# Kernel tuning notes

Measured on AMD Instinct MI355X. Metric: run time of the kernel, lower is better.

Reference implementation:

```python
import jax, jax.numpy as jnp
import numpy as np

EPS = 1e-4


def setup_inputs() -> dict:
    key = jax.random.key(0)
    k1, k2, k3 = jax.random.split(key, 3)
    B, L, M, D = 4, 8192, 4096, 1024
    hidden_states = jax.random.normal(k1, (B, M, D), dtype=jnp.float32)
    boundary_mask = (jax.random.uniform(k2, (B, L)) < 0.45).at[:, 0].set(True)
    boundary_prob = jax.nn.softmax(jax.random.normal(k3, (B, L, 2)), axis=-1)
    mask = jnp.ones((B, L), dtype=bool)
    return {
        "hidden_states": hidden_states,
        "boundary_prob": boundary_prob,
        "boundary_mask": boundary_mask,
        "mask": mask,
    }


def _dechunk(hidden_states, boundary_prob, boundary_mask):
    B, M, D = hidden_states.shape
    L = boundary_mask.shape[1]
    # stable-sort boundary tokens to the front (argsort of offset token idx)
    p_full = jnp.clip(boundary_prob[..., -1].astype(jnp.float32), EPS, 1.0 - EPS)  # [B,L]
    token_idx = jnp.arange(L, dtype=jnp.int32)[None, :] + (~boundary_mask).astype(jnp.int32) * L
    seq_sorted = jnp.argsort(token_idx, axis=1)[:, :M]  # [B,M]
    p = jnp.take_along_axis(p_full, seq_sorted, axis=1)  # [B,M]

    dt = jnp.log(1.0 / (1.0 - p)).astype(jnp.bfloat16)  # bf16 as in module dtype
    x = (hidden_states / dt[..., None].astype(jnp.float32)).astype(jnp.bfloat16)  # [B,M,D]

    # mamba_chunk_scan_combined with A=-1, dstate=1, B=p, C=1 reduces to the
    # linear recurrence h_t = exp(-dt_t) * h_{t-1} + dt_t * p_t * x_t ; y_t = h_t
    dt_f = dt.astype(jnp.float32)
    a = jnp.exp(-dt_f)[..., None]  # [B,M,1] decay = (1-p)
    b = (dt_f * p)[..., None] * x.astype(jnp.float32)  # [B,M,D]

    def combine(e1, e2):
        a1, b1 = e1
        a2, b2 = e2
        return (a1 * a2, a2 * b1 + b2)

    _, h = jax.lax.associative_scan(combine, (a, b), axis=1)  # h: [B,M,D]
    out = h.astype(jnp.bfloat16)  # kernel output dtype follows x (bf16)

    # scatter back: every token reads the state of its (most recent) chunk
    plug_back_idx = jnp.clip(jnp.cumsum(boundary_mask.astype(jnp.int32), axis=1) - 1, 0, M - 1)  # [B,L]
    out_full = jnp.take_along_axis(out, plug_back_idx[..., None], axis=1)  # [B,L,D]
    return out_full.astype(jnp.float32)  # back to original dtype


def reference(hidden_states, boundary_prob, boundary_mask, mask):
    # mask only participates in an assertion in the torch module
    return _dechunk(hidden_states, boundary_prob, boundary_mask)
```

## Files before the change

kernel.cpp:

```cpp
#include <hip/hip_runtime.h>
#include <hip/hip_bf16.h>
#include <math.h>

#define B_ 4
#define L_ 8192
#define M_ 4096
#define D_ 1024
#define CHUNK_ 32
#define NCC_ 128
#define EPS_ 1e-4f

typedef float f32x4 __attribute__((ext_vector_type(4)));

__device__ __forceinline__ float bf16rf(float x) {
  unsigned u = __float_as_uint(x);
  u += 0x7FFFu + ((u >> 16) & 1u);
  u &= 0xFFFF0000u;
  return __uint_as_float(u);
}

__device__ __forceinline__ bool mask_at(const void* mb, int fmt, int i) {
  if (fmt == 0) return ((const unsigned char*)mb)[i] != 0;
  if (fmt == 1) return ((const int*)mb)[i] != 0;
  return ((const float*)mb)[i] != 0.0f;
}

__device__ __forceinline__ void chunk_scal(const float* __restrict__ p_sorted,
                                           int b, int c, int tid,
                                           float4* s_scal) {
  if (tid < CHUNK_) {
    float p = p_sorted[b * M_ + c * CHUNK_ + tid];
    p = fminf(fmaxf(p, EPS_), 1.0f - EPS_);
    float dtf = bf16rf(logf(1.0f / (1.0f - p)));
    s_scal[tid] = make_float4(expf(-dtf), dtf * p, 1.0f / dtf, 0.0f);
  }
}

__global__ void __launch_bounds__(1024)
k_prep(const float* __restrict__ bprob,
       const void* __restrict__ bmask,
       float* __restrict__ p_sorted,
       int* __restrict__ rowstart) {
  const int b = blockIdx.x;
  const int tid = threadIdx.x;
  const int lane = tid & 63, wid = tid >> 6;
  __shared__ int s_flags[2];
  __shared__ int s_wsum[17];

  if (tid < 2) s_flags[tid] = 0;
  __syncthreads();
  {
    const unsigned* mw = (const unsigned*)bmask;
    unsigned f0 = 0, f1 = 0;
    for (int i = tid; i < 8192; i += 1024) {
      unsigned v = mw[i];
      f0 |= v & 0xFFu;
      f1 |= v & 0xFF00u;
    }
    if (f1) s_flags[0] = 1;
    if (f0) s_flags[1] = 1;
  }
  __syncthreads();
  const int fmt = s_flags[0] ? 0 : (s_flags[1] ? 1 : 2);

  const int base_l = tid * (L_ / 1024);
  bool mloc[L_ / 1024];
  int cnt = 0;
#pragma unroll
  for (int j = 0; j < L_ / 1024; ++j) {
    mloc[j] = mask_at(bmask, fmt, b * L_ + base_l + j);
    cnt += mloc[j] ? 1 : 0;
  }
  int incl = cnt;
#pragma unroll
  for (int off = 1; off < 64; off <<= 1) {
    int t = __shfl_up(incl, off);
    if (lane >= off) incl += t;
  }
  if (lane == 63) s_wsum[wid] = incl;
  __syncthreads();
  if (tid == 0) {
    int acc = 0;
#pragma unroll
    for (int w = 0; w < 16; ++w) { int t = s_wsum[w]; s_wsum[w] = acc; acc += t; }
    s_wsum[16] = acc;
  }
  for (int r = tid; r <= M_; r += 1024) rowstart[b * (M_ + 1) + r] = L_;
  __syncthreads();
  const int excl = s_wsum[wid] + incl - cnt;
  const int nb = s_wsum[16];

  int run = excl;
#pragma unroll
  for (int j = 0; j < L_ / 1024; ++j) {
    int l = base_l + j;
    bool mb = mloc[j];
    int pos = mb ? run : (nb + (l - run));
    run += mb ? 1 : 0;
    if (pos < M_) {
      p_sorted[b * M_ + pos] = bprob[((size_t)(b * L_ + l)) * 2 + 1];
      if (mb) rowstart[b * (M_ + 1) + pos] = l;
    }
  }
}

__global__ void __launch_bounds__(256)
k_scanA(const float* __restrict__ hidden,
        const float* __restrict__ p_sorted,
        const int* __restrict__ rowstart,
        float* __restrict__ carry,
        float* __restrict__ Achunk) {
  const int c = blockIdx.x, b = blockIdx.y;
  const int tid = threadIdx.x;
  if (rowstart[b * (M_ + 1) + c * CHUNK_] >= L_) return;
  __shared__ float4 s_scal[CHUNK_];
  chunk_scal(p_sorted, b, c, tid, s_scal);
  __syncthreads();
  if (tid == 0) {
    float cp = 1.0f;
#pragma unroll
    for (int m = 0; m < CHUNK_; ++m) cp *= s_scal[m].x;
    Achunk[b * NCC_ + c] = cp;
  }
  const int d4 = tid * 4;
  const float* __restrict__ hp =
      hidden + ((size_t)(b * M_ + c * CHUNK_)) * D_ + d4;
  float hx = 0.f, hy = 0.f, hz = 0.f, hw = 0.f;
#pragma unroll
  for (int m = 0; m < CHUNK_; ++m) {
    const float4 s = s_scal[m];
    const float4 x = *(const float4*)(hp + (size_t)m * D_);
    hx = fmaf(s.x, hx, s.y * bf16rf(x.x * s.z));
    hy = fmaf(s.x, hy, s.y * bf16rf(x.y * s.z));
    hz = fmaf(s.x, hz, s.y * bf16rf(x.z * s.z));
    hw = fmaf(s.x, hw, s.y * bf16rf(x.w * s.z));
  }
  *(float4*)(carry + ((size_t)(b * NCC_ + c)) * D_ + d4) =
      make_float4(hx, hy, hz, hw);
}

__global__ void __launch_bounds__(64)
k_scanB(float* __restrict__ carry, const float* __restrict__ Achunk) {
  const int chain = blockIdx.x * 64 + threadIdx.x;
  const int bb = chain >> 10, dd = chain & 1023;
  const float* __restrict__ Ab = Achunk + bb * NCC_;
  float S = 0.0f;
  for (int g = 0; g < NCC_ / 16; ++g) {
    float v[16], A[16];
#pragma unroll
    for (int j = 0; j < 16; ++j)
      v[j] = carry[((size_t)(bb * NCC_ + g * 16 + j)) * D_ + dd];
#pragma unroll
    for (int j = 0; j < 16; ++j) A[j] = Ab[g * 16 + j];
#pragma unroll
    for (int j = 0; j < 16; ++j) { S = fmaf(A[j], S, v[j]); v[j] = S; }
#pragma unroll
    for (int j = 0; j < 16; ++j)
      carry[((size_t)(bb * NCC_ + g * 16 + j)) * D_ + dd] = v[j];
  }
}

__global__ void __launch_bounds__(256)
k_scanC(const float* __restrict__ hidden,
        const float* __restrict__ p_sorted,
        const int* __restrict__ rowstart,
        const float* __restrict__ carry,
        float* __restrict__ out) {
  const int c = blockIdx.x, b = blockIdx.y;
  const int tid = threadIdx.x;
  const int d4 = tid * 4;
  __shared__ float4 s_scal[CHUNK_];
  __shared__ int    s_rs[CHUNK_ + 1];

  float hx = 0.f, hy = 0.f, hz = 0.f, hw = 0.f;
  if (c > 0) {
    const float4 ci =
        *(const float4*)(carry + ((size_t)(b * NCC_ + c - 1)) * D_ + d4);
    hx = ci.x; hy = ci.y; hz = ci.z; hw = ci.w;
  }
  chunk_scal(p_sorted, b, c, tid, s_scal);
  if (tid <= CHUNK_) s_rs[tid] = rowstart[b * (M_ + 1) + c * CHUNK_ + tid];
  __syncthreads();
  if (s_rs[0] >= L_) return;

  const float* __restrict__ hp =
      hidden + ((size_t)(b * M_ + c * CHUNK_)) * D_ + d4;
#pragma unroll
  for (int m = 0; m < CHUNK_; ++m) {
    const float4 s = s_scal[m];
    const float4 x = *(const float4*)(hp + (size_t)m * D_);
    hx = fmaf(s.x, hx, s.y * bf16rf(x.x * s.z));
    hy = fmaf(s.x, hy, s.y * bf16rf(x.y * s.z));
    hz = fmaf(s.x, hz, s.y * bf16rf(x.z * s.z));
    hw = fmaf(s.x, hw, s.y * bf16rf(x.w * s.z));
    const int r0 = s_rs[m], r1 = s_rs[m + 1];
    if (r1 > r0) {
      f32x4 o;
      o.x = bf16rf(hx); o.y = bf16rf(hy);
      o.z = bf16rf(hz); o.w = bf16rf(hw);
      for (int l = r0; l < r1; ++l)
        __builtin_nontemporal_store(
            o, (f32x4*)(out + ((size_t)(b * L_ + l)) * D_ + d4));
    }
  }
}

extern "C" void kernel_launch(void* const* d_in, const int* in_sizes, int n_in,
                              void* d_out, int out_size, void* d_ws, size_t ws_size,
                              hipStream_t stream) {
  const float* hidden = (const float*)d_in[0];
  const float* bprob  = (const float*)d_in[1];
  const void*  bmask  = d_in[2];
  float* out = (float*)d_out;

  float* p_sorted = (float*)d_ws;
  float* carry    = p_sorted + B_ * M_;
  float* Achunk   = carry + (size_t)B_ * NCC_ * D_;
  int*   rowstart = (int*)(Achunk + B_ * NCC_);

  k_prep<<<dim3(B_), dim3(1024), 0, stream>>>(bprob, bmask, p_sorted, rowstart);
  k_scanA<<<dim3(NCC_, B_), dim3(256), 0, stream>>>(hidden, p_sorted, rowstart,
                                                    carry, Achunk);
  k_scanB<<<dim3(64), dim3(64), 0, stream>>>(carry, Achunk);
  k_scanC<<<dim3(NCC_, B_), dim3(256), 0, stream>>>(hidden, p_sorted, rowstart,
                                                    carry, out);
}
```

Before: 69.09 us.

## Fuse chunk-carry scan into scanA via last-arriving-block ticket counter

Merges the per-chunk carry computation and the cross-chunk sequential scan into one kernel. Blocks take a ticket from a global atomic counter, and the last 64 blocks to arrive spin-wait until every block has finished, then each runs one slice of the serial carry scan. This removes one kernel launch and its gap, at the cost of a memset, atomic traffic, and spin-waiting. Inactive chunks now also take a ticket so the count stays complete.

```diff
diff --git a/kernel.cpp b/kernel.cpp
--- a/kernel.cpp
+++ b/kernel.cpp
@@ -9,6 +9,9 @@
 #define CHUNK_ 32
 #define NCC_ 128
 #define EPS_ 1e-4f
+#define GRID_AB (NCC_ * B_)
+#define WORKERS_ 64
+#define AGENT __HIP_MEMORY_SCOPE_AGENT
 
 typedef float f32x4 __attribute__((ext_vector_type(4)));
 
@@ -105,58 +108,82 @@
 }
 
 __global__ void __launch_bounds__(256)
-k_scanA(const float* __restrict__ hidden,
-        const float* __restrict__ p_sorted,
-        const int* __restrict__ rowstart,
-        float* __restrict__ carry,
-        float* __restrict__ Achunk) {
+k_scanAB(const float* __restrict__ hidden,
+         const float* __restrict__ p_sorted,
+         const int* __restrict__ rowstart,
+         float* __restrict__ carry,
+         float* __restrict__ Achunk,
+         unsigned* __restrict__ counter) {
   const int c = blockIdx.x, b = blockIdx.y;
   const int tid = threadIdx.x;
-  if (rowstart[b * (M_ + 1) + c * CHUNK_] >= L_) return;
   __shared__ float4 s_scal[CHUNK_];
-  chunk_scal(p_sorted, b, c, tid, s_scal);
-  __syncthreads();
+  __shared__ unsigned s_ticket;
+  const bool active = (rowstart[b * (M_ + 1) + c * CHUNK_] < L_);
+
+  if (active) {
+    chunk_scal(p_sorted, b, c, tid, s_scal);
+    __syncthreads();
+    if (tid == 0) {
+      float cp = 1.0f;
+#pragma unroll
+      for (int m = 0; m < CHUNK_; ++m) cp *= s_scal[m].x;
+      __hip_atomic_store(&Achunk[b * NCC_ + c], cp, __ATOMIC_RELAXED, AGENT);
+    }
+    const int d4 = tid * 4;
+    const float* __restrict__ hp =
+        hidden + ((size_t)(b * M_ + c * CHUNK_)) * D_ + d4;
+    float hx = 0.f, hy = 0.f, hz = 0.f, hw = 0.f;
+#pragma unroll
+    for (int m = 0; m < CHUNK_; ++m) {
+      const float4 s = s_scal[m];
+      const float4 x = *(const float4*)(hp + (size_t)m * D_);
+      hx = fmaf(s.x, hx, s.y * bf16rf(x.x * s.z));
+      hy = fmaf(s.x, hy, s.y * bf16rf(x.y * s.z));
+      hz = fmaf(s.x, hz, s.y * bf16rf(x.z * s.z));
+      hw = fmaf(s.x, hw, s.y * bf16rf(x.w * s.z));
+    }
+    float* cp_ = carry + ((size_t)(b * NCC_ + c)) * D_ + d4;
+    __hip_atomic_store(cp_ + 0, hx, __ATOMIC_RELAXED, AGENT);
+    __hip_atomic_store(cp_ + 1, hy, __ATOMIC_RELAXED, AGENT);
+    __hip_atomic_store(cp_ + 2, hz, __ATOMIC_RELAXED, AGENT);
+    __hip_atomic_store(cp_ + 3, hw, __ATOMIC_RELAXED, AGENT);
+  }
+  __syncthreads();
+  if (tid == 0)
+    s_ticket = __hip_atomic_fetch_add(counter, 1u, __ATOMIC_ACQ_REL, AGENT);
+  __syncthreads();
+  const unsigned ticket = s_ticket;
+  if (ticket < (unsigned)(GRID_AB - WORKERS_)) return;
+
   if (tid == 0) {
-    float cp = 1.0f;
-#pragma unroll
-    for (int m = 0; m < CHUNK_; ++m) cp *= s_scal[m].x;
-    Achunk[b * NCC_ + c] = cp;
-  }
-  const int d4 = tid * 4;
-  const float* __restrict__ hp =
-      hidden + ((size_t)(b * M_ + c * CHUNK_)) * D_ + d4;
-  float hx = 0.f, hy = 0.f, hz = 0.f, hw = 0.f;
-#pragma unroll
-  for (int m = 0; m < CHUNK_; ++m) {
-    const float4 s = s_scal[m];
-    const float4 x = *(const float4*)(hp + (size_t)m * D_);
-    hx = fmaf(s.x, hx, s.y * bf16rf(x.x * s.z));
-    hy = fmaf(s.x, hy, s.y * bf16rf(x.y * s.z));
-    hz = fmaf(s.x, hz, s.y * bf16rf(x.z * s.z));
-    hw = fmaf(s.x, hw, s.y * bf16rf(x.w * s.z));
-  }
-  *(float4*)(carry + ((size_t)(b * NCC_ + c)) * D_ + d4) =
-      make_float4(hx, hy, hz, hw);
-}
-
-__global__ void __launch_bounds__(64)
-k_scanB(float* __restrict__ carry, const float* __restrict__ Achunk) {
-  const int chain = blockIdx.x * 64 + threadIdx.x;
-  const int bb = chain >> 10, dd = chain & 1023;
-  const float* __restrict__ Ab = Achunk + bb * NCC_;
-  float S = 0.0f;
-  for (int g = 0; g < NCC_ / 16; ++g) {
-    float v[16], A[16];
-#pragma unroll
-    for (int j = 0; j < 16; ++j)
-      v[j] = carry[((size_t)(bb * NCC_ + g * 16 + j)) * D_ + dd];
-#pragma unroll
-    for (int j = 0; j < 16; ++j) A[j] = Ab[g * 16 + j];
-#pragma unroll
-    for (int j = 0; j < 16; ++j) { S = fmaf(A[j], S, v[j]); v[j] = S; }
-#pragma unroll
-    for (int j = 0; j < 16; ++j)
-      carry[((size_t)(bb * NCC_ + g * 16 + j)) * D_ + dd] = v[j];
+    while (__hip_atomic_load(counter, __ATOMIC_ACQUIRE, AGENT) <
+           (unsigned)GRID_AB)
+      __builtin_amdgcn_s_sleep(2);
+  }
+  __syncthreads();
+  if (tid < 64) {
+    const int chain = (int)(ticket - (GRID_AB - WORKERS_)) * 64 + tid;
+    const int bb = chain >> 10, dd = chain & 1023;
+    float S = 0.0f;
+    for (int g = 0; g < NCC_ / 16; ++g) {
+      float v[16], A[16];
+#pragma unroll
+      for (int j = 0; j < 16; ++j)
+        v[j] = __hip_atomic_load(
+            &carry[((size_t)(bb * NCC_ + g * 16 + j)) * D_ + dd],
+            __ATOMIC_RELAXED, AGENT);
+#pragma unroll
+      for (int j = 0; j < 16; ++j)
+        A[j] = __hip_atomic_load(&Achunk[bb * NCC_ + g * 16 + j],
+                                 __ATOMIC_RELAXED, AGENT);
+#pragma unroll
+      for (int j = 0; j < 16; ++j) { S = fmaf(A[j], S, v[j]); v[j] = S; }
+#pragma unroll
+      for (int j = 0; j < 16; ++j)
+        __hip_atomic_store(
+            &carry[((size_t)(bb * NCC_ + g * 16 + j)) * D_ + dd], v[j],
+            __ATOMIC_RELAXED, AGENT);
+    }
   }
 }
 
@@ -168,6 +195,7 @@
         float* __restrict__ out) {
   const int c = blockIdx.x, b = blockIdx.y;
   const int tid = threadIdx.x;
+  if (rowstart[b * (M_ + 1) + c * CHUNK_] >= L_) return;
   const int d4 = tid * 4;
   __shared__ float4 s_scal[CHUNK_];
   __shared__ int    s_rs[CHUNK_ + 1];
@@ -181,7 +209,6 @@
   chunk_scal(p_sorted, b, c, tid, s_scal);
   if (tid <= CHUNK_) s_rs[tid] = rowstart[b * (M_ + 1) + c * CHUNK_ + tid];
   __syncthreads();
-  if (s_rs[0] >= L_) return;
 
   const float* __restrict__ hp =
       hidden + ((size_t)(b * M_ + c * CHUNK_)) * D_ + d4;
@@ -213,15 +240,16 @@
   const void*  bmask  = d_in[2];
   float* out = (float*)d_out;
 
-  float* p_sorted = (float*)d_ws;
-  float* carry    = p_sorted + B_ * M_;
-  float* Achunk   = carry + (size_t)B_ * NCC_ * D_;
-  int*   rowstart = (int*)(Achunk + B_ * NCC_);
-
+  float*    p_sorted = (float*)d_ws;
+  float*    carry    = p_sorted + B_ * M_;
+  float*    Achunk   = carry + (size_t)B_ * NCC_ * D_;
+  int*      rowstart = (int*)(Achunk + B_ * NCC_);
+  unsigned* counter  = (unsigned*)(rowstart + B_ * (M_ + 1));
+
+  hipMemsetAsync((void*)counter, 0, sizeof(unsigned), stream);
   k_prep<<<dim3(B_), dim3(1024), 0, stream>>>(bprob, bmask, p_sorted, rowstart);
-  k_scanA<<<dim3(NCC_, B_), dim3(256), 0, stream>>>(hidden, p_sorted, rowstart,
-                                                    carry, Achunk);
-  k_scanB<<<dim3(64), dim3(64), 0, stream>>>(carry, Achunk);
+  k_scanAB<<<dim3(NCC_, B_), dim3(256), 0, stream>>>(hidden, p_sorted, rowstart,
+                                                     carry, Achunk, counter);
   k_scanC<<<dim3(NCC_, B_), dim3(256), 0, stream>>>(hidden, p_sorted, rowstart,
                                                     carry, out);
 }
```

Result: slower. 86.55 us (+25.3%).

## Fuse carry-propagation scan into output kernel via device-scope counter

Applied to the files above, without the earlier changes.

Merges the serial inter-chunk carry scan into the final output kernel. The first 16 blocks perform the carry chains and signal completion with an agent-scope atomic counter, and the other blocks spin on that counter before reading their incoming carry. This removes one kernel launch and its drain gap, and lets blocks prefetch their per-chunk scalars while the carry scan runs. It relies on the 16 worker blocks being scheduled before the waiting blocks, and it adds spin-wait and atomic traffic. Waiting blocks also cannot start their main loop until every carry chain has finished.

```diff
diff --git a/kernel.cpp b/kernel.cpp
--- a/kernel.cpp
+++ b/kernel.cpp
@@ -9,6 +9,8 @@
 #define CHUNK_ 32
 #define NCC_ 128
 #define EPS_ 1e-4f
+#define NWORK_ 16
+#define AGENT __HIP_MEMORY_SCOPE_AGENT
 
 typedef float f32x4 __attribute__((ext_vector_type(4)));
 
@@ -40,13 +42,15 @@
 k_prep(const float* __restrict__ bprob,
        const void* __restrict__ bmask,
        float* __restrict__ p_sorted,
-       int* __restrict__ rowstart) {
+       int* __restrict__ rowstart,
+       unsigned* __restrict__ counter) {
   const int b = blockIdx.x;
   const int tid = threadIdx.x;
   const int lane = tid & 63, wid = tid >> 6;
   __shared__ int s_flags[2];
   __shared__ int s_wsum[17];
 
+  if (b == 0 && tid == 0) *counter = 0u;
   if (tid < 2) s_flags[tid] = 0;
   __syncthreads();
   {
@@ -139,49 +143,66 @@
       make_float4(hx, hy, hz, hw);
 }
 
-__global__ void __launch_bounds__(64)
-k_scanB(float* __restrict__ carry, const float* __restrict__ Achunk) {
-  const int chain = blockIdx.x * 64 + threadIdx.x;
-  const int bb = chain >> 10, dd = chain & 1023;
-  const float* __restrict__ Ab = Achunk + bb * NCC_;
-  float S = 0.0f;
-  for (int g = 0; g < NCC_ / 16; ++g) {
-    float v[16], A[16];
-#pragma unroll
-    for (int j = 0; j < 16; ++j)
-      v[j] = carry[((size_t)(bb * NCC_ + g * 16 + j)) * D_ + dd];
-#pragma unroll
-    for (int j = 0; j < 16; ++j) A[j] = Ab[g * 16 + j];
-#pragma unroll
-    for (int j = 0; j < 16; ++j) { S = fmaf(A[j], S, v[j]); v[j] = S; }
-#pragma unroll
-    for (int j = 0; j < 16; ++j)
-      carry[((size_t)(bb * NCC_ + g * 16 + j)) * D_ + dd] = v[j];
-  }
-}
-
 __global__ void __launch_bounds__(256)
-k_scanC(const float* __restrict__ hidden,
-        const float* __restrict__ p_sorted,
-        const int* __restrict__ rowstart,
-        const float* __restrict__ carry,
-        float* __restrict__ out) {
-  const int c = blockIdx.x, b = blockIdx.y;
+k_scanBC(const float* __restrict__ hidden,
+         const float* __restrict__ p_sorted,
+         const int* __restrict__ rowstart,
+         float* __restrict__ carry,
+         const float* __restrict__ Achunk,
+         unsigned* __restrict__ counter,
+         float* __restrict__ out) {
+  const int bx = blockIdx.x;
+  const int c = bx & (NCC_ - 1), b = bx >> 7;
   const int tid = threadIdx.x;
-  const int d4 = tid * 4;
+
+  if (bx < NWORK_) {
+    const int chain = bx * 256 + tid;
+    const int bb = chain >> 10, dd = chain & 1023;
+    const float* __restrict__ Ab = Achunk + bb * NCC_;
+    float S = 0.0f;
+    for (int g = 0; g < NCC_ / 16; ++g) {
+      float v[16], A[16];
+#pragma unroll
+      for (int j = 0; j < 16; ++j)
+        v[j] = carry[((size_t)(bb * NCC_ + g * 16 + j)) * D_ + dd];
+#pragma unroll
+      for (int j = 0; j < 16; ++j) A[j] = Ab[g * 16 + j];
+#pragma unroll
+      for (int j = 0; j < 16; ++j) { S = fmaf(A[j], S, v[j]); v[j] = S; }
+#pragma unroll
+      for (int j = 0; j < 16; ++j)
+        __hip_atomic_store(
+            &carry[((size_t)(bb * NCC_ + g * 16 + j)) * D_ + dd], v[j],
+            __ATOMIC_RELAXED, AGENT);
+    }
+    __syncthreads();
+    if (tid == 0)
+      __hip_atomic_fetch_add(counter, 1u, __ATOMIC_ACQ_REL, AGENT);
+  }
+
   __shared__ float4 s_scal[CHUNK_];
   __shared__ int    s_rs[CHUNK_ + 1];
-
+  chunk_scal(p_sorted, b, c, tid, s_scal);
+  if (tid <= CHUNK_) s_rs[tid] = rowstart[b * (M_ + 1) + c * CHUNK_ + tid];
+  __syncthreads();
+  if (s_rs[0] >= L_) return;
+
+  const int d4 = tid * 4;
   float hx = 0.f, hy = 0.f, hz = 0.f, hw = 0.f;
   if (c > 0) {
-    const float4 ci =
-        *(const float4*)(carry + ((size_t)(b * NCC_ + c - 1)) * D_ + d4);
-    hx = ci.x; hy = ci.y; hz = ci.z; hw = ci.w;
-  }
-  chunk_scal(p_sorted, b, c, tid, s_scal);
-  if (tid <= CHUNK_) s_rs[tid] = rowstart[b * (M_ + 1) + c * CHUNK_ + tid];
-  __syncthreads();
-  if (s_rs[0] >= L_) return;
+    if (tid == 0) {
+      while (__hip_atomic_load(counter, __ATOMIC_RELAXED, AGENT) <
+             (unsigned)NWORK_)
+        __builtin_amdgcn_s_sleep(2);
+    }
+    __syncthreads();
+    __builtin_amdgcn_fence(__ATOMIC_ACQUIRE, "agent");
+    const float* ip = carry + ((size_t)(b * NCC_ + c - 1)) * D_ + d4;
+    hx = __hip_atomic_load(ip + 0, __ATOMIC_RELAXED, AGENT);
+    hy = __hip_atomic_load(ip + 1, __ATOMIC_RELAXED, AGENT);
+    hz = __hip_atomic_load(ip + 2, __ATOMIC_RELAXED, AGENT);
+    hw = __hip_atomic_load(ip + 3, __ATOMIC_RELAXED, AGENT);
+  }
 
   const float* __restrict__ hp =
       hidden + ((size_t)(b * M_ + c * CHUNK_)) * D_ + d4;
@@ -213,15 +234,16 @@
   const void*  bmask  = d_in[2];
   float* out = (float*)d_out;
 
-  float* p_sorted = (float*)d_ws;
-  float* carry    = p_sorted + B_ * M_;
-  float* Achunk   = carry + (size_t)B_ * NCC_ * D_;
-  int*   rowstart = (int*)(Achunk + B_ * NCC_);
-
-  k_prep<<<dim3(B_), dim3(1024), 0, stream>>>(bprob, bmask, p_sorted, rowstart);
+  float*    p_sorted = (float*)d_ws;
+  float*    carry    = p_sorted + B_ * M_;
+  float*    Achunk   = carry + (size_t)B_ * NCC_ * D_;
+  int*      rowstart = (int*)(Achunk + B_ * NCC_);
+  unsigned* counter  = (unsigned*)(rowstart + B_ * (M_ + 1));
+
+  k_prep<<<dim3(B_), dim3(1024), 0, stream>>>(bprob, bmask, p_sorted, rowstart,
+                                              counter);
   k_scanA<<<dim3(NCC_, B_), dim3(256), 0, stream>>>(hidden, p_sorted, rowstart,
                                                     carry, Achunk);
-  k_scanB<<<dim3(64), dim3(64), 0, stream>>>(carry, Achunk);
-  k_scanC<<<dim3(NCC_, B_), dim3(256), 0, stream>>>(hidden, p_sorted, rowstart,
-                                                    carry, out);
-}
+  k_scanBC<<<dim3(NCC_ * B_), dim3(256), 0, stream>>>(hidden, p_sorted, rowstart,
+                                                      carry, Achunk, counter, out);
+}
```

New measurement: 81.79 us. 1.18x slower.
